# Optimization experiments

Hardware: AMD Instinct MI355X
Metric: run time of the kernel (lower is better)

Reference implementation:

```python
import jax, jax.numpy as jnp
import numpy as np

HEADS = 8
EMB = 128

def setup_inputs() -> dict:
    key = jax.random.key(0)
    ks = jax.random.split(key, 5)
    b, t, hin = 4, 128, 1024
    N = 50000
    x = jax.random.normal(ks[0], (b, t, hin), dtype=jnp.float32)
    curiosity_score = jax.random.normal(ks[1], (b, t), dtype=jnp.float32)
    Wq = jax.random.normal(ks[2], (EMB * HEADS, hin), dtype=jnp.float32) * (1.0 / np.sqrt(hin))
    keys = jax.random.normal(ks[3], (N, EMB), dtype=jnp.float32)
    values = jax.random.normal(ks[4], (N,), dtype=jnp.float32)
    return {"x": x, "curiosity_score": curiosity_score, "Wq": Wq, "keys": keys, "values": values}

def reference(x, curiosity_score, Wq, keys, values):
    b, t, hin = x.shape
    h, e = HEADS, EMB
    # query projection (torch Linear, no bias): x @ Wq.T -> (b, t, h*e)
    q = jnp.einsum('bti,oi->bto', x, Wq).reshape(b, t, h, e)
    q = q / (e ** 0.25)
    # scores vs shared offline key bank (N, e); buffer was `heads` identical copies,
    # so broadcasting over h is the same math without materializing repeats.
    scores = jnp.einsum('bthe,ne->bthn', q, keys)          # (b, t, h, N)
    attn = jax.nn.softmax(scores, axis=-1)
    # weighted sum of scalar values; curiosity adds a per-query constant to every
    # value, and since attn rows sum to 1 this equals adding curiosity afterwards.
    out = jnp.einsum('bthn,n->bth', attn, values) + curiosity_score[:, :, None]
    out = out.mean(axis=2)                                  # mean over heads
    return out[:, :, None]                                  # (b, t, 1)
```

## Files before the change

kernel.cpp:

```cpp
#include <hip/hip_runtime.h>

#define NHEADS   8
#define EMB_     128
#define BT_      512
#define HIN_     1024
#define NQ_      4096
#define NKEY_    50000
#define NGRP_REAL_ 3125
#define NGRP_    3200
#define NPADKEYS_ 1200.0f
#define GPS_     50
#define NSLICES_ 64

#define PROJB_   512
#define CONVB_   1024

#define QSCALE   (0.29730177875068026f * 1.4426950408889634f)

typedef __attribute__((ext_vector_type(8))) short short8v;
typedef __attribute__((ext_vector_type(4))) float float4v;

#if __has_builtin(__builtin_amdgcn_exp2f)
#define EXP2F(x) __builtin_amdgcn_exp2f(x)
#else
#define EXP2F(x) exp2f(x)
#endif

__device__ __forceinline__ short f2bf(float f) {
  unsigned u = __float_as_uint(f);
  u += 0x7fffu + ((u >> 16) & 1u);
  return (short)(u >> 16);
}

#if __has_builtin(__builtin_amdgcn_cvt_pk_bf16_f32)
typedef __attribute__((ext_vector_type(2))) __bf16 bf16x2;
__device__ __forceinline__ unsigned pk2(float a, float b) {
  bf16x2 r = __builtin_amdgcn_cvt_pk_bf16_f32(a, b);
  union { bf16x2 v; unsigned u; } c; c.v = r; return c.u;
}
#else
__device__ __forceinline__ unsigned pk2(float a, float b) {
  unsigned r;
  asm("v_cvt_pk_bf16_f32 %0, %1, %2" : "=v"(r) : "v"(a), "v"(b));
  return r;
}
#endif

__global__ __launch_bounds__(256) void prep_kernel(
    const float* __restrict__ x, const float* __restrict__ Wq,
    short* __restrict__ qb,
    const float* __restrict__ keys, const float* __restrict__ values,
    short* __restrict__ keys_fr, float* __restrict__ vpad) {
  if (blockIdx.x < PROJB_) {
    const int wave = threadIdx.x >> 6, lane = threadIdx.x & 63;
    const int quad = lane >> 4, ln = lane & 15;
    const int tile = blockIdx.x * 4 + wave;
    const int mt = tile >> 6, ot = tile & 63;
    const float* xrow = x  + (mt * 16 + ln) * HIN_ + quad * 8;
    const float* wrow = Wq + (ot * 16 + ln) * HIN_ + quad * 8;
    float4v d = {0.f, 0.f, 0.f, 0.f};

    float4 xa0 = *(const float4*)(xrow);
    float4 xa1 = *(const float4*)(xrow + 4);
    float4 wa0 = *(const float4*)(wrow);
    float4 wa1 = *(const float4*)(wrow + 4);
    float4 xb0 = *(const float4*)(xrow + 32);
    float4 xb1 = *(const float4*)(xrow + 36);
    float4 wb0 = *(const float4*)(wrow + 32);
    float4 wb1 = *(const float4*)(wrow + 36);

#pragma unroll 1
    for (int k0 = 0; k0 < HIN_; k0 += 64) {
      union { short8v s8; unsigned u[4]; } af, bf;
      af.u[0] = pk2(xa0.x, xa0.y); af.u[1] = pk2(xa0.z, xa0.w);
      af.u[2] = pk2(xa1.x, xa1.y); af.u[3] = pk2(xa1.z, xa1.w);
      bf.u[0] = pk2(wa0.x, wa0.y); bf.u[1] = pk2(wa0.z, wa0.w);
      bf.u[2] = pk2(wa1.x, wa1.y); bf.u[3] = pk2(wa1.z, wa1.w);
      if (k0 + 64 < HIN_) {
        xa0 = *(const float4*)(xrow + k0 + 64);
        xa1 = *(const float4*)(xrow + k0 + 68);
        wa0 = *(const float4*)(wrow + k0 + 64);
        wa1 = *(const float4*)(wrow + k0 + 68);
      }
      d = __builtin_amdgcn_mfma_f32_16x16x32_bf16(af.s8, bf.s8, d, 0, 0, 0);

      af.u[0] = pk2(xb0.x, xb0.y); af.u[1] = pk2(xb0.z, xb0.w);
      af.u[2] = pk2(xb1.x, xb1.y); af.u[3] = pk2(xb1.z, xb1.w);
      bf.u[0] = pk2(wb0.x, wb0.y); bf.u[1] = pk2(wb0.z, wb0.w);
      bf.u[2] = pk2(wb1.x, wb1.y); bf.u[3] = pk2(wb1.z, wb1.w);
      if (k0 + 96 < HIN_) {
        xb0 = *(const float4*)(xrow + k0 + 96);
        xb1 = *(const float4*)(xrow + k0 + 100);
        wb0 = *(const float4*)(wrow + k0 + 96);
        wb1 = *(const float4*)(wrow + k0 + 100);
      }
      d = __builtin_amdgcn_mfma_f32_16x16x32_bf16(af.s8, bf.s8, d, 0, 0, 0);
    }
#pragma unroll
    for (int r2 = 0; r2 < 4; ++r2)
      qb[(mt * 16 + quad * 4 + r2) * HIN_ + ot * 16 + ln] = f2bf(d[r2] * QSCALE);
  } else {
    const int cb = blockIdx.x - PROJB_;
    const int t  = threadIdx.x;
#pragma unroll 1
    for (int g = cb; g < NGRP_; g += CONVB_) {
      if (g < NGRP_REAL_) {
        const float* src = keys + (g * 16 + (t & 15)) * EMB_ + (t >> 4) * 8;
        float4 v0 = ((const float4*)src)[0];
        float4 v1 = ((const float4*)src)[1];
        union { short8v s8; unsigned u[4]; } o;
        o.u[0] = pk2(v0.x, v0.y); o.u[1] = pk2(v0.z, v0.w);
        o.u[2] = pk2(v1.x, v1.y); o.u[3] = pk2(v1.z, v1.w);
        ((short8v*)keys_fr)[g * 256 + t] = o.s8;
        if (t < 16) vpad[g * 16 + t] = values[g * 16 + t];
      } else {
        short8v z = (short8v)0;
        ((short8v*)keys_fr)[g * 256 + t] = z;
        if (t < 16) vpad[g * 16 + t] = 0.f;
      }
    }
  }
}

__global__ __launch_bounds__(256) void attn_kernel(
    const short* __restrict__ qb,
    const short* __restrict__ keys_fr,
    const float* __restrict__ vpad,
    float* __restrict__ partials) {
  const int t     = threadIdx.x;
  const int wave  = t >> 6;
  const int lane  = t & 63;
  const int quad  = lane >> 4;
  const int ln    = lane & 15;
  const int l     = blockIdx.x;
  const int xcd   = l & 7;
  const int j     = l >> 3;
  const int slice = xcd * 8 + (j >> 4);
  const int chunk = j & 15;
  const int qbase = chunk * 256 + wave * 64;
  const int g0    = slice * GPS_;
  const int g1    = g0 + GPS_;

  short8v a[4][4];
#pragma unroll
  for (int sub = 0; sub < 4; ++sub)
#pragma unroll
    for (int ks = 0; ks < 4; ++ks)
      a[sub][ks] = *(const short8v*)(qb + (qbase + sub * 16 + ln) * EMB_ + ks * 32 + quad * 8);

  float lsum[4][4], asum[4][4];
#pragma unroll
  for (int i = 0; i < 4; ++i)
#pragma unroll
    for (int jj = 0; jj < 4; ++jj) { lsum[i][jj] = 0.f; asum[i][jj] = 0.f; }

  const float4v z4 = {0.f, 0.f, 0.f, 0.f};

  short8v bA[4], bB[4];
  float vA, vB;
#pragma unroll
  for (int ks = 0; ks < 4; ++ks)
    bA[ks] = *(const short8v*)(keys_fr + ((g0 * 4 + ks) * 64 + lane) * 8);
  vA = vpad[g0 * 16 + ln];
#pragma unroll
  for (int ks = 0; ks < 4; ++ks)
    bB[ks] = *(const short8v*)(keys_fr + (((g0 + 1) * 4 + ks) * 64 + lane) * 8);
  vB = vpad[(g0 + 1) * 16 + ln];

#pragma unroll 1
  for (int g = g0; g < g1; g += 2) {
    float4v dE[4];
    __builtin_amdgcn_s_setprio(1);
#pragma unroll
    for (int sub = 0; sub < 4; ++sub)
      dE[sub] = __builtin_amdgcn_mfma_f32_16x16x32_bf16(a[sub][0], bA[0], z4, 0, 0, 0);
#pragma unroll
    for (int ks = 1; ks < 4; ++ks)
#pragma unroll
      for (int sub = 0; sub < 4; ++sub)
        dE[sub] = __builtin_amdgcn_mfma_f32_16x16x32_bf16(a[sub][ks], bA[ks], dE[sub], 0, 0, 0);
    __builtin_amdgcn_s_setprio(0);
    if (g + 2 < g1) {
#pragma unroll
      for (int ks = 0; ks < 4; ++ks)
        bA[ks] = *(const short8v*)(keys_fr + (((g + 2) * 4 + ks) * 64 + lane) * 8);
    }
    float vvA = vA;
    if (g + 2 < g1) vA = vpad[(g + 2) * 16 + ln];

#pragma unroll
    for (int sub = 0; sub < 4; ++sub)
#pragma unroll
      for (int r2 = 0; r2 < 4; ++r2) {
        float pE = EXP2F(dE[sub][r2]);
        lsum[sub][r2] += pE;
        asum[sub][r2] = fmaf(pE, vvA, asum[sub][r2]);
      }

    float4v dO[4];
    __builtin_amdgcn_s_setprio(1);
#pragma unroll
    for (int sub = 0; sub < 4; ++sub)
      dO[sub] = __builtin_amdgcn_mfma_f32_16x16x32_bf16(a[sub][0], bB[0], z4, 0, 0, 0);
#pragma unroll
    for (int ks = 1; ks < 4; ++ks)
#pragma unroll
      for (int sub = 0; sub < 4; ++sub)
        dO[sub] = __builtin_amdgcn_mfma_f32_16x16x32_bf16(a[sub][ks], bB[ks], dO[sub], 0, 0, 0);
    __builtin_amdgcn_s_setprio(0);
    if (g + 3 < g1) {
#pragma unroll
      for (int ks = 0; ks < 4; ++ks)
        bB[ks] = *(const short8v*)(keys_fr + (((g + 3) * 4 + ks) * 64 + lane) * 8);
    }
    float vvB = vB;
    if (g + 3 < g1) vB = vpad[(g + 3) * 16 + ln];

#pragma unroll
    for (int sub = 0; sub < 4; ++sub)
#pragma unroll
      for (int r2 = 0; r2 < 4; ++r2) {
        float pO = EXP2F(dO[sub][r2]);
        lsum[sub][r2] += pO;
        asum[sub][r2] = fmaf(pO, vvB, asum[sub][r2]);
      }
  }

#pragma unroll
  for (int sub = 0; sub < 4; ++sub)
#pragma unroll
    for (int r2 = 0; r2 < 4; ++r2) {
      float L = lsum[sub][r2], A = asum[sub][r2];
#pragma unroll
      for (int m = 1; m < 16; m <<= 1) {
        L += __shfl_xor(L, m, 64);
        A += __shfl_xor(A, m, 64);
      }
      if (ln == 0) {
        int q = qbase + sub * 16 + quad * 4 + r2;
        partials[(q * NSLICES_ + slice) * 2 + 0] = L;
        partials[(q * NSLICES_ + slice) * 2 + 1] = A;
      }
    }
}

__global__ __launch_bounds__(256) void finalize_kernel(
    const float* __restrict__ partials, const float* __restrict__ cur,
    float* __restrict__ out) {
  int tid = blockIdx.x * 256 + threadIdx.x;
  int bt = tid >> 3, h = tid & 7;
  int q = bt * NHEADS + h;
  const float4* p = (const float4*)(partials + q * NSLICES_ * 2);
  float sl = 0.f, sa = 0.f;
#pragma unroll
  for (int i = 0; i < NSLICES_ / 2; ++i) {
    float4 v = p[i];
    sl += v.x + v.z;
    sa += v.y + v.w;
  }
  sl -= NPADKEYS_;
  float r = sa / sl;
  r += __shfl_xor(r, 1, 64);
  r += __shfl_xor(r, 2, 64);
  r += __shfl_xor(r, 4, 64);
  if (h == 0) out[bt] = r * (1.f / NHEADS) + cur[bt];
}

extern "C" void kernel_launch(void* const* d_in, const int* in_sizes, int n_in,
                              void* d_out, int out_size, void* d_ws, size_t ws_size,
                              hipStream_t stream) {
  (void)in_sizes; (void)n_in; (void)out_size; (void)ws_size;
  const float* x      = (const float*)d_in[0];
  const float* cur    = (const float*)d_in[1];
  const float* Wq     = (const float*)d_in[2];
  const float* keys   = (const float*)d_in[3];
  const float* values = (const float*)d_in[4];
  float* out = (float*)d_out;

  char* ws = (char*)d_ws;
  short* keys_fr = (short*)(ws);
  float* vpad    = (float*)(ws + 13107200);
  short* qb      = (short*)(ws + 13312000);
  float* part    = (float*)(ws + 14360576);

  hipLaunchKernelGGL(prep_kernel, dim3(PROJB_ + CONVB_), dim3(256), 0, stream,
                     x, Wq, qb, keys, values, keys_fr, vpad);
  hipLaunchKernelGGL(attn_kernel, dim3(1024), dim3(256), 0, stream,
                     qb, keys_fr, vpad, part);
  hipLaunchKernelGGL(finalize_kernel, dim3(16), dim3(256), 0, stream, part, cur, out);
}
```

Before: 174.6 us.

## Stage key tiles through double-buffered LDS with async global-to-LDS loads

```diff
diff --git a/kernel.cpp b/kernel.cpp
--- a/kernel.cpp
+++ b/kernel.cpp
@@ -10,6 +10,7 @@
 #define NGRP_    3200
 #define NPADKEYS_ 1200.0f
 #define GPS_     50
+#define NTILES_  25
 #define NSLICES_ 64
 
 #define PROJB_   512
@@ -45,6 +46,12 @@
   return r;
 }
 #endif
+
+__device__ __forceinline__ void gload_lds16(const short* g, short* l) {
+  __builtin_amdgcn_global_load_lds(
+      (const __attribute__((address_space(1))) unsigned int*)g,
+      (__attribute__((address_space(3))) unsigned int*)l, 16, 0, 0);
+}
 
 __global__ __launch_bounds__(256) void prep_kernel(
     const float* __restrict__ x, const float* __restrict__ Wq,
@@ -127,6 +134,7 @@
     const short* __restrict__ keys_fr,
     const float* __restrict__ vpad,
     float* __restrict__ partials) {
+  __shared__ short kbuf[2][4096];
   const int t     = threadIdx.x;
   const int wave  = t >> 6;
   const int lane  = t & 63;
@@ -139,7 +147,8 @@
   const int chunk = j & 15;
   const int qbase = chunk * 256 + wave * 64;
   const int g0    = slice * GPS_;
-  const int g1    = g0 + GPS_;
+
+  const short* gkey = keys_fr + g0 * 2048;
 
   short8v a[4][4];
 #pragma unroll
@@ -156,21 +165,34 @@
 
   const float4v z4 = {0.f, 0.f, 0.f, 0.f};
 
-  short8v bA[4], bB[4];
-  float vA, vB;
-#pragma unroll
-  for (int ks = 0; ks < 4; ++ks)
-    bA[ks] = *(const short8v*)(keys_fr + ((g0 * 4 + ks) * 64 + lane) * 8);
-  vA = vpad[g0 * 16 + ln];
-#pragma unroll
-  for (int ks = 0; ks < 4; ++ks)
-    bB[ks] = *(const short8v*)(keys_fr + (((g0 + 1) * 4 + ks) * 64 + lane) * 8);
-  vB = vpad[(g0 + 1) * 16 + ln];
-
+  gload_lds16(gkey + wave * 512 + lane * 8, &kbuf[0][wave * 512]);
+  gload_lds16(gkey + 2048 + wave * 512 + lane * 8, &kbuf[0][2048 + wave * 512]);
+  float vA = vpad[g0 * 16 + ln];
+  float vB = vpad[(g0 + 1) * 16 + ln];
+  asm volatile("s_waitcnt vmcnt(0)");
+  __syncthreads();
+
+  int buf = 0;
 #pragma unroll 1
-  for (int g = g0; g < g1; g += 2) {
+  for (int p = 0; p < NTILES_; ++p) {
+    const int g = g0 + 2 * p;
+    if (p + 1 < NTILES_) {
+      const short* gp = gkey + (2 * p + 2) * 2048 + wave * 512 + lane * 8;
+      short* lp = &kbuf[buf ^ 1][wave * 512];
+      gload_lds16(gp, lp);
+      gload_lds16(gp + 2048, lp + 2048);
+    }
+
+    const short* kb = kbuf[buf];
+    short8v bA[4], bB[4];
+#pragma unroll
+    for (int ks = 0; ks < 4; ++ks)
+      bA[ks] = *(const short8v*)(kb + (ks * 64 + lane) * 8);
+#pragma unroll
+    for (int ks = 0; ks < 4; ++ks)
+      bB[ks] = *(const short8v*)(kb + 2048 + (ks * 64 + lane) * 8);
+
     float4v dE[4];
-    __builtin_amdgcn_s_setprio(1);
 #pragma unroll
     for (int sub = 0; sub < 4; ++sub)
       dE[sub] = __builtin_amdgcn_mfma_f32_16x16x32_bf16(a[sub][0], bA[0], z4, 0, 0, 0);
@@ -179,14 +201,8 @@
 #pragma unroll
       for (int sub = 0; sub < 4; ++sub)
         dE[sub] = __builtin_amdgcn_mfma_f32_16x16x32_bf16(a[sub][ks], bA[ks], dE[sub], 0, 0, 0);
-    __builtin_amdgcn_s_setprio(0);
-    if (g + 2 < g1) {
-#pragma unroll
-      for (int ks = 0; ks < 4; ++ks)
-        bA[ks] = *(const short8v*)(keys_fr + (((g + 2) * 4 + ks) * 64 + lane) * 8);
-    }
     float vvA = vA;
-    if (g + 2 < g1) vA = vpad[(g + 2) * 16 + ln];
+    if (p + 1 < NTILES_) vA = vpad[(g + 2) * 16 + ln];
 
 #pragma unroll
     for (int sub = 0; sub < 4; ++sub)
@@ -198,7 +214,6 @@
       }
 
     float4v dO[4];
-    __builtin_amdgcn_s_setprio(1);
 #pragma unroll
     for (int sub = 0; sub < 4; ++sub)
       dO[sub] = __builtin_amdgcn_mfma_f32_16x16x32_bf16(a[sub][0], bB[0], z4, 0, 0, 0);
@@ -207,14 +222,8 @@
 #pragma unroll
       for (int sub = 0; sub < 4; ++sub)
         dO[sub] = __builtin_amdgcn_mfma_f32_16x16x32_bf16(a[sub][ks], bB[ks], dO[sub], 0, 0, 0);
-    __builtin_amdgcn_s_setprio(0);
-    if (g + 3 < g1) {
-#pragma unroll
-      for (int ks = 0; ks < 4; ++ks)
-        bB[ks] = *(const short8v*)(keys_fr + (((g + 3) * 4 + ks) * 64 + lane) * 8);
-    }
     float vvB = vB;
-    if (g + 3 < g1) vB = vpad[(g + 3) * 16 + ln];
+    if (p + 1 < NTILES_) vB = vpad[(g + 3) * 16 + ln];
 
 #pragma unroll
     for (int sub = 0; sub < 4; ++sub)
@@ -224,6 +233,9 @@
         lsum[sub][r2] += pO;
         asum[sub][r2] = fmaf(pO, vvB, asum[sub][r2]);
       }
+
+    __syncthreads();
+    buf ^= 1;
   }
 
 #pragma unroll
```

After: 177.8 us. No clear change (+1.8%).

## Fuse finalize into attention via last-block ticket and use packed FP32 accumulation

Applied to the files above, without the earlier changes.

```diff
diff --git a/kernel.cpp b/kernel.cpp
--- a/kernel.cpp
+++ b/kernel.cpp
@@ -19,6 +19,7 @@
 
 typedef __attribute__((ext_vector_type(8))) short short8v;
 typedef __attribute__((ext_vector_type(4))) float float4v;
+typedef __attribute__((ext_vector_type(2))) float float2v;
 
 #if __has_builtin(__builtin_amdgcn_exp2f)
 #define EXP2F(x) __builtin_amdgcn_exp2f(x)
@@ -26,6 +27,13 @@
 #define EXP2F(x) exp2f(x)
 #endif
 
+__device__ __forceinline__ void pk_add(float2v& acc, float2v p) {
+  asm("v_pk_add_f32 %0, %1, %0" : "+v"(acc) : "v"(p));
+}
+__device__ __forceinline__ void pk_fma(float2v& acc, float2v p, float2v v) {
+  asm("v_pk_fma_f32 %0, %1, %2, %0" : "+v"(acc) : "v"(p), "v"(v));
+}
+
 __device__ __forceinline__ short f2bf(float f) {
   unsigned u = __float_as_uint(f);
   u += 0x7fffu + ((u >> 16) & 1u);
@@ -50,7 +58,8 @@
     const float* __restrict__ x, const float* __restrict__ Wq,
     short* __restrict__ qb,
     const float* __restrict__ keys, const float* __restrict__ values,
-    short* __restrict__ keys_fr, float* __restrict__ vpad) {
+    short* __restrict__ keys_fr, float* __restrict__ vpad,
+    unsigned* __restrict__ ticket) {
   if (blockIdx.x < PROJB_) {
     const int wave = threadIdx.x >> 6, lane = threadIdx.x & 63;
     const int quad = lane >> 4, ln = lane & 15;
@@ -119,6 +128,8 @@
         if (t < 16) vpad[g * 16 + t] = 0.f;
       }
     }
+    const int idx = cb * 256 + t;
+    if (idx < 16) ticket[idx] = 0u;
   }
 }
 
@@ -126,7 +137,10 @@
     const short* __restrict__ qb,
     const short* __restrict__ keys_fr,
     const float* __restrict__ vpad,
-    float* __restrict__ partials) {
+    float* __restrict__ partials,
+    unsigned* __restrict__ ticket,
+    const float* __restrict__ cur,
+    float* __restrict__ out) {
   const int t     = threadIdx.x;
   const int wave  = t >> 6;
   const int lane  = t & 63;
@@ -148,11 +162,14 @@
     for (int ks = 0; ks < 4; ++ks)
       a[sub][ks] = *(const short8v*)(qb + (qbase + sub * 16 + ln) * EMB_ + ks * 32 + quad * 8);
 
-  float lsum[4][4], asum[4][4];
+  float2v lsum[4][2], asum[4][2];
 #pragma unroll
   for (int i = 0; i < 4; ++i)
 #pragma unroll
-    for (int jj = 0; jj < 4; ++jj) { lsum[i][jj] = 0.f; asum[i][jj] = 0.f; }
+    for (int h = 0; h < 2; ++h) {
+      lsum[i][h] = (float2v){0.f, 0.f};
+      asum[i][h] = (float2v){0.f, 0.f};
+    }
 
   const float4v z4 = {0.f, 0.f, 0.f, 0.f};
 
@@ -187,15 +204,17 @@
     }
     float vvA = vA;
     if (g + 2 < g1) vA = vpad[(g + 2) * 16 + ln];
-
-#pragma unroll
-    for (int sub = 0; sub < 4; ++sub)
-#pragma unroll
-      for (int r2 = 0; r2 < 4; ++r2) {
-        float pE = EXP2F(dE[sub][r2]);
-        lsum[sub][r2] += pE;
-        asum[sub][r2] = fmaf(pE, vvA, asum[sub][r2]);
-      }
+    float2v vvA2 = {vvA, vvA};
+
+#pragma unroll
+    for (int sub = 0; sub < 4; ++sub) {
+      float2v p01 = {EXP2F(dE[sub][0]), EXP2F(dE[sub][1])};
+      float2v p23 = {EXP2F(dE[sub][2]), EXP2F(dE[sub][3])};
+      pk_add(lsum[sub][0], p01);
+      pk_add(lsum[sub][1], p23);
+      pk_fma(asum[sub][0], p01, vvA2);
+      pk_fma(asum[sub][1], p23, vvA2);
+    }
 
     float4v dO[4];
     __builtin_amdgcn_s_setprio(1);
@@ -215,55 +234,60 @@
     }
     float vvB = vB;
     if (g + 3 < g1) vB = vpad[(g + 3) * 16 + ln];
-
-#pragma unroll
-    for (int sub = 0; sub < 4; ++sub)
-#pragma unroll
-      for (int r2 = 0; r2 < 4; ++r2) {
-        float pO = EXP2F(dO[sub][r2]);
-        lsum[sub][r2] += pO;
-        asum[sub][r2] = fmaf(pO, vvB, asum[sub][r2]);
+    float2v vvB2 = {vvB, vvB};
+
+#pragma unroll
+    for (int sub = 0; sub < 4; ++sub) {
+      float2v p01 = {EXP2F(dO[sub][0]), EXP2F(dO[sub][1])};
+      float2v p23 = {EXP2F(dO[sub][2]), EXP2F(dO[sub][3])};
+      pk_add(lsum[sub][0], p01);
+      pk_add(lsum[sub][1], p23);
+      pk_fma(asum[sub][0], p01, vvB2);
+      pk_fma(asum[sub][1], p23, vvB2);
+    }
+  }
+
+#pragma unroll
+  for (int sub = 0; sub < 4; ++sub)
+#pragma unroll
+    for (int h = 0; h < 2; ++h)
+#pragma unroll
+      for (int jj = 0; jj < 2; ++jj) {
+        float L = lsum[sub][h][jj], A = asum[sub][h][jj];
+#pragma unroll
+        for (int m = 1; m < 16; m <<= 1) {
+          L += __shfl_xor(L, m, 64);
+          A += __shfl_xor(A, m, 64);
+        }
+        if (ln == 0) {
+          int q = qbase + sub * 16 + quad * 4 + h * 2 + jj;
+          partials[(q * NSLICES_ + slice) * 2 + 0] = L;
+          partials[(q * NSLICES_ + slice) * 2 + 1] = A;
+        }
       }
+
+  __threadfence();
+  __shared__ int amLast;
+  if (t == 0) amLast = (atomicAdd(&ticket[chunk], 1u) == 63u);
+  __syncthreads();
+  if (amLast) {
+    __threadfence();
+    const int q = chunk * 256 + t;
+    const float4* pp = (const float4*)(partials + q * NSLICES_ * 2);
+    float sl = 0.f, sa = 0.f;
+#pragma unroll
+    for (int i = 0; i < NSLICES_ / 2; ++i) {
+      float4 v = pp[i];
+      sl += v.x + v.z;
+      sa += v.y + v.w;
+    }
+    sl -= NPADKEYS_;
+    float r = sa / sl;
+    r += __shfl_xor(r, 1, 64);
+    r += __shfl_xor(r, 2, 64);
+    r += __shfl_xor(r, 4, 64);
+    if ((t & 7) == 0) out[q >> 3] = r * (1.f / NHEADS) + cur[q >> 3];
   }
-
-#pragma unroll
-  for (int sub = 0; sub < 4; ++sub)
-#pragma unroll
-    for (int r2 = 0; r2 < 4; ++r2) {
-      float L = lsum[sub][r2], A = asum[sub][r2];
-#pragma unroll
-      for (int m = 1; m < 16; m <<= 1) {
-        L += __shfl_xor(L, m, 64);
-        A += __shfl_xor(A, m, 64);
-      }
-      if (ln == 0) {
-        int q = qbase + sub * 16 + quad * 4 + r2;
-        partials[(q * NSLICES_ + slice) * 2 + 0] = L;
-        partials[(q * NSLICES_ + slice) * 2 + 1] = A;
-      }
-    }
-}
-
-__global__ __launch_bounds__(256) void finalize_kernel(
-    const float* __restrict__ partials, const float* __restrict__ cur,
-    float* __restrict__ out) {
-  int tid = blockIdx.x * 256 + threadIdx.x;
-  int bt = tid >> 3, h = tid & 7;
-  int q = bt * NHEADS + h;
-  const float4* p = (const float4*)(partials + q * NSLICES_ * 2);
-  float sl = 0.f, sa = 0.f;
-#pragma unroll
-  for (int i = 0; i < NSLICES_ / 2; ++i) {
-    float4 v = p[i];
-    sl += v.x + v.z;
-    sa += v.y + v.w;
-  }
-  sl -= NPADKEYS_;
-  float r = sa / sl;
-  r += __shfl_xor(r, 1, 64);
-  r += __shfl_xor(r, 2, 64);
-  r += __shfl_xor(r, 4, 64);
-  if (h == 0) out[bt] = r * (1.f / NHEADS) + cur[bt];
 }
 
 extern "C" void kernel_launch(void* const* d_in, const int* in_sizes, int n_in,
@@ -278,14 +302,14 @@
   float* out = (float*)d_out;
 
   char* ws = (char*)d_ws;
-  short* keys_fr = (short*)(ws);
-  float* vpad    = (float*)(ws + 13107200);
-  short* qb      = (short*)(ws + 13312000);
-  float* part    = (float*)(ws + 14360576);
+  short* keys_fr   = (short*)(ws);
+  float* vpad      = (float*)(ws + 13107200);
+  short* qb        = (short*)(ws + 13312000);
+  float* part      = (float*)(ws + 14360576);
+  unsigned* ticket = (unsigned*)(ws + 16457728);
 
   hipLaunchKernelGGL(prep_kernel, dim3(PROJB_ + CONVB_), dim3(256), 0, stream,
-                     x, Wq, qb, keys, values, keys_fr, vpad);
+                     x, Wq, qb, keys, values, keys_fr, vpad, ticket);
   hipLaunchKernelGGL(attn_kernel, dim3(1024), dim3(256), 0, stream,
-                     qb, keys_fr, vpad, part);
-  hipLaunchKernelGGL(finalize_kernel, dim3(16), dim3(256), 0, stream, part, cur, out);
-}
+                     qb, keys_fr, vpad, part, ticket, cur, out);
+}
```

Measured after the change: 266.4 us. 52.6% more time.
